# Kernel optimization log

Hardware: AMD Instinct MI355X
Metric: run time of the kernel (lower is better)

Reference implementation:

```python
import jax, jax.numpy as jnp
import numpy as np

N_NODES = 100000
N_EDGES = 1600000


def _sage_conv(x, src, dst, W_neigh, W_self, b, n_nodes):
    # mean aggregation over in-neighbors (dst receives from src), DGL 'mean' SAGEConv
    agg = jax.ops.segment_sum(x[src], dst, num_segments=n_nodes)          # [N, d]
    deg = jax.ops.segment_sum(jnp.ones((src.shape[0],), x.dtype), dst,
                              num_segments=n_nodes)                        # [N]
    mean = agg / jnp.maximum(deg, 1.0)[:, None]
    return x @ W_self + mean @ W_neigh + b


def setup_inputs() -> dict:
    key = jax.random.key(0)
    ks = jax.random.split(key, 10)
    d_in, d_hid, d_out = 64, 64, 32
    x = jax.random.normal(ks[0], (N_NODES, d_in), jnp.float32)
    src = jax.random.randint(ks[1], (N_EDGES,), 0, N_NODES, jnp.int32)
    dst = jax.random.randint(ks[2], (N_EDGES,), 0, N_NODES, jnp.int32)
    def w(k, i, o):
        return jax.random.normal(k, (i, o), jnp.float32) / np.sqrt(i)
    return {
        "x": x, "src": src, "dst": dst,
        "W_self1": w(ks[3], d_in, d_hid), "W_neigh1": w(ks[4], d_in, d_hid),
        "b1": jnp.zeros((d_hid,), jnp.float32),
        "W_self2": w(ks[5], d_hid, d_hid), "W_neigh2": w(ks[6], d_hid, d_hid),
        "b2": jnp.zeros((d_hid,), jnp.float32),
        "W_self3": w(ks[7], d_hid, d_out), "W_neigh3": w(ks[8], d_hid, d_out),
        "b3": jnp.zeros((d_out,), jnp.float32),
    }


def reference(x, src, dst, W_self1, W_neigh1, b1, W_self2, W_neigh2, b2,
              W_self3, W_neigh3, b3):
    n = x.shape[0]
    h = _sage_conv(x, src, dst, W_neigh1, W_self1, b1, n)
    h = _sage_conv(h, src, dst, W_neigh2, W_self2, b2, n)
    h = _sage_conv(h, src, dst, W_neigh3, W_self3, b3, n)
    h = jax.nn.relu(h)
    # Dropout(0.5) treated in eval mode (identity) for deterministic reference
    return h
```

## Files before the change

### kernel.cpp

```cpp
#include <hip/hip_runtime.h>


#define NN 100000
#define NE 1600000
#define GEMM_BLOCKS 1024


__global__ __launch_bounds__(256) void deg_count_kernel(
    const int* __restrict__ dst, int* __restrict__ deg, int n_edges) {
  int e = blockIdx.x * 256 + threadIdx.x;
  if (e < n_edges) atomicAdd(&deg[dst[e]], 1);
}

__global__ __launch_bounds__(256) void scan_partial_kernel(
    const int* __restrict__ deg, int* __restrict__ partials, int n_nodes) {
  __shared__ int sb[256];
  int t = threadIdx.x;
  int i = blockIdx.x * 256 + t;
  sb[t] = (i < n_nodes) ? deg[i] : 0;
  __syncthreads();
  for (int off = 128; off > 0; off >>= 1) {
    if (t < off) sb[t] += sb[t + off];
    __syncthreads();
  }
  if (t == 0) partials[blockIdx.x] = sb[0];
}

__global__ __launch_bounds__(512) void scan_top_kernel(
    int* __restrict__ partials, int nb, int* __restrict__ rowp, int n_nodes) {
  __shared__ int tmp[512];
  int t = threadIdx.x;
  int v = (t < nb) ? partials[t] : 0;
  tmp[t] = v;
  __syncthreads();
  for (int off = 1; off < 512; off <<= 1) {
    int add = (t >= off) ? tmp[t - off] : 0;
    __syncthreads();
    tmp[t] += add;
    __syncthreads();
  }
  if (t < nb) partials[t] = tmp[t] - v;
  if (t == 511) rowp[n_nodes] = tmp[511];
}

__global__ __launch_bounds__(256) void scan_final_kernel(
    const int* __restrict__ deg, const int* __restrict__ partials,
    int* __restrict__ rowp, int* __restrict__ cursor,
    float* __restrict__ degf, int n_nodes) {
  __shared__ int tmp[256];
  int t = threadIdx.x;
  int i = blockIdx.x * 256 + t;
  int v = (i < n_nodes) ? deg[i] : 0;
  tmp[t] = v;
  __syncthreads();
  for (int off = 1; off < 256; off <<= 1) {
    int add = (t >= off) ? tmp[t - off] : 0;
    __syncthreads();
    tmp[t] += add;
    __syncthreads();
  }
  if (i < n_nodes) {
    int exc = tmp[t] - v + partials[blockIdx.x];
    rowp[i] = exc;
    cursor[i] = exc;
    degf[i] = fmaxf((float)v, 1.0f);
  }
}

__global__ __launch_bounds__(256) void fill_kernel(
    const int* __restrict__ src, const int* __restrict__ dst,
    int* __restrict__ cursor, int* __restrict__ col, int n_edges) {
  int e = blockIdx.x * 256 + threadIdx.x;
  if (e < n_edges) {
    int pos = atomicAdd(&cursor[dst[e]], 1);
    col[pos] = src[e];
  }
}


__global__ __launch_bounds__(256) void agg_mean_kernel(
    const float* __restrict__ h_in,
    const int* __restrict__ rowp,
    const int* __restrict__ col,
    const float* __restrict__ degf,
    float* __restrict__ mean_out) {
  const int tid  = threadIdx.x;
  const int wave = tid >> 6;
  const int lane = tid & 63;
  const int g    = lane >> 4;
  const int f4   = (lane & 15) * 4;

  const int n = blockIdx.x * 16 + wave * 4 + g;

  const int e0 = rowp[n];
  const int e1 = rowp[n + 1];
  const int ecount = e1 - e0;

  float4 acc = {0.f, 0.f, 0.f, 0.f};
  int e = 0;
  for (; e + 8 <= ecount; e += 8) {
    int i0 = col[e0 + e + 0], i1 = col[e0 + e + 1];
    int i2 = col[e0 + e + 2], i3 = col[e0 + e + 3];
    int i4 = col[e0 + e + 4], i5 = col[e0 + e + 5];
    int i6 = col[e0 + e + 6], i7 = col[e0 + e + 7];
    float4 v0 = *(const float4*)(h_in + (size_t)i0 * 64 + f4);
    float4 v1 = *(const float4*)(h_in + (size_t)i1 * 64 + f4);
    float4 v2 = *(const float4*)(h_in + (size_t)i2 * 64 + f4);
    float4 v3 = *(const float4*)(h_in + (size_t)i3 * 64 + f4);
    float4 v4 = *(const float4*)(h_in + (size_t)i4 * 64 + f4);
    float4 v5 = *(const float4*)(h_in + (size_t)i5 * 64 + f4);
    float4 v6 = *(const float4*)(h_in + (size_t)i6 * 64 + f4);
    float4 v7 = *(const float4*)(h_in + (size_t)i7 * 64 + f4);
    acc.x += ((v0.x + v1.x) + (v2.x + v3.x)) + ((v4.x + v5.x) + (v6.x + v7.x));
    acc.y += ((v0.y + v1.y) + (v2.y + v3.y)) + ((v4.y + v5.y) + (v6.y + v7.y));
    acc.z += ((v0.z + v1.z) + (v2.z + v3.z)) + ((v4.z + v5.z) + (v6.z + v7.z));
    acc.w += ((v0.w + v1.w) + (v2.w + v3.w)) + ((v4.w + v5.w) + (v6.w + v7.w));
  }
  if (e < ecount) {
    const int last = e1 - 1;
#pragma unroll
    for (int u = 0; u < 8; ++u) {
      int ee = e0 + e + u;
      int ii = col[ee <= last ? ee : last];
      float4 v = *(const float4*)(h_in + (size_t)ii * 64 + f4);
      float msk = (e + u < ecount) ? 1.0f : 0.0f;
      acc.x = fmaf(v.x, msk, acc.x);
      acc.y = fmaf(v.y, msk, acc.y);
      acc.z = fmaf(v.z, msk, acc.z);
      acc.w = fmaf(v.w, msk, acc.w);
    }
  }

  const float d = degf[n];
  float4 mv = {acc.x / d, acc.y / d, acc.z / d, acc.w / d};
  *(float4*)(mean_out + (size_t)n * 64 + f4) = mv;
}


template <int DOUT, bool RELU>
__global__ __launch_bounds__(256) void gemm_kernel(
    const float* __restrict__ h_self,
    const float* __restrict__ mean,
    const float* __restrict__ Wself,
    const float* __restrict__ Wneigh,
    const float* __restrict__ bias,
    float* __restrict__ h_out) {
  __shared__ float Wt[DOUT][132];
  __shared__ float rowbuf[4][128];

  const int tid  = threadIdx.x;
  const int wave = tid >> 6;
  const int lane = tid & 63;

  for (int idx = tid; idx < DOUT * 128; idx += 256) {
    int c = idx & (DOUT - 1);
    int k = idx / DOUT;
    Wt[c][k] = (k < 64) ? Wself[k * DOUT + c] : Wneigh[(k - 64) * DOUT + c];
  }
  __syncthreads();

  const float bval = (lane < DOUT) ? bias[lane] : 0.0f;

  for (int gblk = blockIdx.x; gblk < NN / 4; gblk += GEMM_BLOCKS) {
    const int n = gblk * 4 + wave;
    rowbuf[wave][lane]      = h_self[(size_t)n * 64 + lane];
    rowbuf[wave][64 + lane] = mean[(size_t)n * 64 + lane];

    if (lane < DOUT) {
      float o0 = 0.f, o1 = 0.f, o2 = 0.f, o3 = 0.f;
#pragma unroll
      for (int j = 0; j < 32; ++j) {
        const float4 w = *(const float4*)&Wt[lane][j * 4];
        const float4 r = *(const float4*)&rowbuf[wave][j * 4];
        o0 = fmaf(r.x, w.x, o0);
        o1 = fmaf(r.y, w.y, o1);
        o2 = fmaf(r.z, w.z, o2);
        o3 = fmaf(r.w, w.w, o3);
      }
      float o = ((o0 + o1) + (o2 + o3)) + bval;
      if (RELU) o = fmaxf(o, 0.0f);
      h_out[(size_t)n * DOUT + lane] = o;
    }
  }
}


extern "C" void kernel_launch(void* const* d_in, const int* in_sizes, int n_in,
                              void* d_out, int out_size, void* d_ws, size_t ws_size,
                              hipStream_t stream) {
  const float* x   = (const float*)d_in[0];
  const int*   src = (const int*)d_in[1];
  const int*   dst = (const int*)d_in[2];
  const float* Ws1 = (const float*)d_in[3];
  const float* Wn1 = (const float*)d_in[4];
  const float* b1  = (const float*)d_in[5];
  const float* Ws2 = (const float*)d_in[6];
  const float* Wn2 = (const float*)d_in[7];
  const float* b2  = (const float*)d_in[8];
  const float* Ws3 = (const float*)d_in[9];
  const float* Wn3 = (const float*)d_in[10];
  const float* b3  = (const float*)d_in[11];
  float* out = (float*)d_out;

  char* ws = (char*)d_ws;
  size_t off = 0;
  auto take = [&](size_t bytes) -> void* {
    void* p = ws + off;
    off += (bytes + 255) & ~(size_t)255;
    return p;
  };
  int*   deg      = (int*)take((size_t)NN * 4);
  float* degf     = (float*)take((size_t)NN * 4);
  int*   rowp     = (int*)take((size_t)(NN + 1) * 4);
  int*   cursor   = (int*)take((size_t)NN * 4);
  int*   partials = (int*)take(1024 * 4);
  int*   col      = (int*)take((size_t)NE * 4);
  float* h1       = (float*)take((size_t)NN * 64 * 4);
  float* h2       = (float*)take((size_t)NN * 64 * 4);
  float* meanbuf  = (float*)take((size_t)NN * 64 * 4);
  (void)ws_size; (void)in_sizes; (void)n_in; (void)out_size;

  hipMemsetAsync(deg, 0, (size_t)NN * 4, stream);

  const int EB = (NE + 255) / 256;
  const int NB = (NN + 255) / 256;
  const int AB = NN / 16;

  deg_count_kernel<<<EB, 256, 0, stream>>>(dst, deg, NE);
  scan_partial_kernel<<<NB, 256, 0, stream>>>(deg, partials, NN);
  scan_top_kernel<<<1, 512, 0, stream>>>(partials, NB, rowp, NN);
  scan_final_kernel<<<NB, 256, 0, stream>>>(deg, partials, rowp, cursor, degf, NN);
  fill_kernel<<<EB, 256, 0, stream>>>(src, dst, cursor, col, NE);

  agg_mean_kernel<<<AB, 256, 0, stream>>>(x, rowp, col, degf, meanbuf);
  gemm_kernel<64, false><<<GEMM_BLOCKS, 256, 0, stream>>>(x, meanbuf, Ws1, Wn1, b1, h1);

  agg_mean_kernel<<<AB, 256, 0, stream>>>(h1, rowp, col, degf, meanbuf);
  gemm_kernel<64, false><<<GEMM_BLOCKS, 256, 0, stream>>>(h1, meanbuf, Ws2, Wn2, b2, h2);

  agg_mean_kernel<<<AB, 256, 0, stream>>>(h2, rowp, col, degf, meanbuf);
  gemm_kernel<32, true ><<<GEMM_BLOCKS, 256, 0, stream>>>(h2, meanbuf, Ws3, Wn3, b3, out);
}
```

Before: 619.9 us.

## Store node features chunk-major so gather passes work on cache-resident slices

Feature matrices are now stored as eight 8-float column chunks (each NN x 8). Aggregation runs as a 2D grid over node blocks and chunks, with two threads per node each gathering a float4 from a 3.2MB slice. The goal is to keep the random neighbour gathers inside L2/LLC instead of striding over the full 25.6MB matrix. The cost is an extra transpose kernel for x, eight passes over the col array per layer, and strided 32-byte accesses in the GEMM loads and stores.

```diff
diff --git a/kernel.cpp b/kernel.cpp
--- a/kernel.cpp
+++ b/kernel.cpp
@@ -4,6 +4,7 @@
 #define NN 100000
 #define NE 1600000
 #define GEMM_BLOCKS 1024
+#define CS ((size_t)NN * 8)
 
 
 __global__ __launch_bounds__(256) void deg_count_kernel(
@@ -78,69 +79,58 @@
 }
 
 
-__global__ __launch_bounds__(256) void agg_mean_kernel(
-    const float* __restrict__ h_in,
+__global__ __launch_bounds__(256) void to_chunk_major_kernel(
+    const float* __restrict__ x, float* __restrict__ xT) {
+  int t = blockIdx.x * 256 + threadIdx.x;
+  int n = t >> 6;
+  int f = t & 63;
+  xT[(size_t)(f >> 3) * CS + (size_t)n * 8 + (f & 7)] = x[t];
+}
+
+
+__global__ __launch_bounds__(256) void agg_chunked_kernel(
+    const float* __restrict__ hT,
     const int* __restrict__ rowp,
     const int* __restrict__ col,
     const float* __restrict__ degf,
-    float* __restrict__ mean_out) {
-  const int tid  = threadIdx.x;
-  const int wave = tid >> 6;
-  const int lane = tid & 63;
-  const int g    = lane >> 4;
-  const int f4   = (lane & 15) * 4;
-
-  const int n = blockIdx.x * 16 + wave * 4 + g;
-
+    float* __restrict__ meanT) {
+  const int p = blockIdx.y;
+  const int n = blockIdx.x * 128 + (threadIdx.x >> 1);
+  const int h = threadIdx.x & 1;
+  if (n >= NN) return;
+
+  const float* base = hT + (size_t)p * CS + (size_t)h * 4;
   const int e0 = rowp[n];
   const int e1 = rowp[n + 1];
-  const int ecount = e1 - e0;
-
-  float4 acc = {0.f, 0.f, 0.f, 0.f};
-  int e = 0;
-  for (; e + 8 <= ecount; e += 8) {
-    int i0 = col[e0 + e + 0], i1 = col[e0 + e + 1];
-    int i2 = col[e0 + e + 2], i3 = col[e0 + e + 3];
-    int i4 = col[e0 + e + 4], i5 = col[e0 + e + 5];
-    int i6 = col[e0 + e + 6], i7 = col[e0 + e + 7];
-    float4 v0 = *(const float4*)(h_in + (size_t)i0 * 64 + f4);
-    float4 v1 = *(const float4*)(h_in + (size_t)i1 * 64 + f4);
-    float4 v2 = *(const float4*)(h_in + (size_t)i2 * 64 + f4);
-    float4 v3 = *(const float4*)(h_in + (size_t)i3 * 64 + f4);
-    float4 v4 = *(const float4*)(h_in + (size_t)i4 * 64 + f4);
-    float4 v5 = *(const float4*)(h_in + (size_t)i5 * 64 + f4);
-    float4 v6 = *(const float4*)(h_in + (size_t)i6 * 64 + f4);
-    float4 v7 = *(const float4*)(h_in + (size_t)i7 * 64 + f4);
-    acc.x += ((v0.x + v1.x) + (v2.x + v3.x)) + ((v4.x + v5.x) + (v6.x + v7.x));
-    acc.y += ((v0.y + v1.y) + (v2.y + v3.y)) + ((v4.y + v5.y) + (v6.y + v7.y));
-    acc.z += ((v0.z + v1.z) + (v2.z + v3.z)) + ((v4.z + v5.z) + (v6.z + v7.z));
-    acc.w += ((v0.w + v1.w) + (v2.w + v3.w)) + ((v4.w + v5.w) + (v6.w + v7.w));
-  }
-  if (e < ecount) {
-    const int last = e1 - 1;
-#pragma unroll
-    for (int u = 0; u < 8; ++u) {
-      int ee = e0 + e + u;
-      int ii = col[ee <= last ? ee : last];
-      float4 v = *(const float4*)(h_in + (size_t)ii * 64 + f4);
-      float msk = (e + u < ecount) ? 1.0f : 0.0f;
-      acc.x = fmaf(v.x, msk, acc.x);
-      acc.y = fmaf(v.y, msk, acc.y);
-      acc.z = fmaf(v.z, msk, acc.z);
-      acc.w = fmaf(v.w, msk, acc.w);
-    }
+
+  float ax = 0.f, ay = 0.f, az = 0.f, aw = 0.f;
+  int e = e0;
+  for (; e + 4 <= e1; e += 4) {
+    int i0 = col[e], i1 = col[e + 1], i2 = col[e + 2], i3 = col[e + 3];
+    float4 v0 = *(const float4*)(base + (size_t)i0 * 8);
+    float4 v1 = *(const float4*)(base + (size_t)i1 * 8);
+    float4 v2 = *(const float4*)(base + (size_t)i2 * 8);
+    float4 v3 = *(const float4*)(base + (size_t)i3 * 8);
+    ax += (v0.x + v1.x) + (v2.x + v3.x);
+    ay += (v0.y + v1.y) + (v2.y + v3.y);
+    az += (v0.z + v1.z) + (v2.z + v3.z);
+    aw += (v0.w + v1.w) + (v2.w + v3.w);
+  }
+  for (; e < e1; ++e) {
+    float4 v = *(const float4*)(base + (size_t)col[e] * 8);
+    ax += v.x; ay += v.y; az += v.z; aw += v.w;
   }
 
   const float d = degf[n];
-  float4 mv = {acc.x / d, acc.y / d, acc.z / d, acc.w / d};
-  *(float4*)(mean_out + (size_t)n * 64 + f4) = mv;
+  float4 mv = {ax / d, ay / d, az / d, aw / d};
+  *(float4*)(meanT + (size_t)p * CS + (size_t)n * 8 + (size_t)h * 4) = mv;
 }
 
 
 template <int DOUT, bool RELU>
 __global__ __launch_bounds__(256) void gemm_kernel(
-    const float* __restrict__ h_self,
-    const float* __restrict__ mean,
+    const float* __restrict__ hT_self,
+    const float* __restrict__ meanT,
     const float* __restrict__ Wself,
     const float* __restrict__ Wneigh,
     const float* __restrict__ bias,
@@ -160,11 +150,12 @@
   __syncthreads();
 
   const float bval = (lane < DOUT) ? bias[lane] : 0.0f;
+  const size_t coff = (size_t)(lane >> 3) * CS + (size_t)(lane & 7);
 
   for (int gblk = blockIdx.x; gblk < NN / 4; gblk += GEMM_BLOCKS) {
     const int n = gblk * 4 + wave;
-    rowbuf[wave][lane]      = h_self[(size_t)n * 64 + lane];
-    rowbuf[wave][64 + lane] = mean[(size_t)n * 64 + lane];
+    rowbuf[wave][lane]      = hT_self[coff + (size_t)n * 8];
+    rowbuf[wave][64 + lane] = meanT[coff + (size_t)n * 8];
 
     if (lane < DOUT) {
       float o0 = 0.f, o1 = 0.f, o2 = 0.f, o3 = 0.f;
@@ -179,7 +170,11 @@
       }
       float o = ((o0 + o1) + (o2 + o3)) + bval;
       if (RELU) o = fmaxf(o, 0.0f);
-      h_out[(size_t)n * DOUT + lane] = o;
+      if (DOUT == 64) {
+        h_out[(size_t)(lane >> 3) * CS + (size_t)n * 8 + (lane & 7)] = o;
+      } else {
+        h_out[(size_t)n * DOUT + lane] = o;
+      }
     }
   }
 }
@@ -215,16 +210,16 @@
   int*   cursor   = (int*)take((size_t)NN * 4);
   int*   partials = (int*)take(1024 * 4);
   int*   col      = (int*)take((size_t)NE * 4);
-  float* h1       = (float*)take((size_t)NN * 64 * 4);
-  float* h2       = (float*)take((size_t)NN * 64 * 4);
-  float* meanbuf  = (float*)take((size_t)NN * 64 * 4);
+  float* bufA     = (float*)take((size_t)NN * 64 * 4);
+  float* bufB     = (float*)take((size_t)NN * 64 * 4);
+  float* meanT    = (float*)take((size_t)NN * 64 * 4);
   (void)ws_size; (void)in_sizes; (void)n_in; (void)out_size;
 
   hipMemsetAsync(deg, 0, (size_t)NN * 4, stream);
 
   const int EB = (NE + 255) / 256;
   const int NB = (NN + 255) / 256;
-  const int AB = NN / 16;
+  const dim3 AG((NN + 127) / 128, 8, 1);
 
   deg_count_kernel<<<EB, 256, 0, stream>>>(dst, deg, NE);
   scan_partial_kernel<<<NB, 256, 0, stream>>>(deg, partials, NN);
@@ -232,12 +227,14 @@
   scan_final_kernel<<<NB, 256, 0, stream>>>(deg, partials, rowp, cursor, degf, NN);
   fill_kernel<<<EB, 256, 0, stream>>>(src, dst, cursor, col, NE);
 
-  agg_mean_kernel<<<AB, 256, 0, stream>>>(x, rowp, col, degf, meanbuf);
-  gemm_kernel<64, false><<<GEMM_BLOCKS, 256, 0, stream>>>(x, meanbuf, Ws1, Wn1, b1, h1);
-
-  agg_mean_kernel<<<AB, 256, 0, stream>>>(h1, rowp, col, degf, meanbuf);
-  gemm_kernel<64, false><<<GEMM_BLOCKS, 256, 0, stream>>>(h1, meanbuf, Ws2, Wn2, b2, h2);
-
-  agg_mean_kernel<<<AB, 256, 0, stream>>>(h2, rowp, col, degf, meanbuf);
-  gemm_kernel<32, true ><<<GEMM_BLOCKS, 256, 0, stream>>>(h2, meanbuf, Ws3, Wn3, b3, out);
-}
+  to_chunk_major_kernel<<<NN * 64 / 256, 256, 0, stream>>>(x, bufA);
+
+  agg_chunked_kernel<<<AG, 256, 0, stream>>>(bufA, rowp, col, degf, meanT);
+  gemm_kernel<64, false><<<GEMM_BLOCKS, 256, 0, stream>>>(bufA, meanT, Ws1, Wn1, b1, bufB);
+
+  agg_chunked_kernel<<<AG, 256, 0, stream>>>(bufB, rowp, col, degf, meanT);
+  gemm_kernel<64, false><<<GEMM_BLOCKS, 256, 0, stream>>>(bufB, meanT, Ws2, Wn2, b2, bufA);
+
+  agg_chunked_kernel<<<AG, 256, 0, stream>>>(bufA, rowp, col, degf, meanT);
+  gemm_kernel<32, true ><<<GEMM_BLOCKS, 256, 0, stream>>>(bufA, meanT, Ws3, Wn3, b3, out);
+}
```

Measured after the change: 892.3 us. 1.44x slower.
